# Performance work log

Measured on AMD Instinct MI355X. Metric: run time of the kernel, lower is better.

The kernel has to match this reference:

```python
import jax, jax.numpy as jnp
import numpy as np

# ---- dims (match init_kwargs / input_specs) ----
N = 50000        # nodes
E = 600000       # edges
F_IN = 128       # n_features
HID = 128        # hidden_dims
K = 8            # heads
D_A = 16         # attention dim per head
D_V = 16         # value dim per head
D_M = 64         # max-pool gate dim
CLASSES = 40     # n_classes
LAYERS = 2
SLOPE = 0.1      # negative_slop


def glorot(key, shape):
    lim = jnp.sqrt(6.0 / (shape[-2] + shape[-1]))
    return jax.random.uniform(key, shape, minval=-lim, maxval=lim, dtype=jnp.float32)


def setup_inputs() -> dict:
    key = jax.random.key(0)
    ks = jax.random.split(key, 10)
    x = jax.random.normal(ks[0], (N, F_IN), dtype=jnp.float32)
    edge_index = jax.random.randint(ks[1], (2, E), 0, N, dtype=jnp.int64)
    weight_in = glorot(ks[2], (F_IN, HID))
    weight_out = glorot(ks[3], (HID, CLASSES))
    # per-layer GaANConv params, stacked on leading layer dim
    Wq = glorot(ks[4], (LAYERS, HID, K * D_A))            # query proj
    Wk = glorot(ks[5], (LAYERS, HID, K * D_A))            # key proj
    Wv = glorot(ks[6], (LAYERS, HID, K * D_V))            # value proj
    Wm = glorot(ks[7], (LAYERS, HID, D_M))                # max-pool gate proj
    Wg = glorot(ks[8], (LAYERS, HID + D_M + HID, K))      # gate FC
    Wo = glorot(ks[9], (LAYERS, HID + K * D_V, HID))      # output proj
    return {"x": x, "edge_index": edge_index, "weight_in": weight_in,
            "weight_out": weight_out, "Wq": Wq, "Wk": Wk, "Wv": Wv,
            "Wm": Wm, "Wg": Wg, "Wo": Wo}


def gaan_conv(x, src, dst, wq, wk, wv, wm, wg, wo):
    n = x.shape[0]
    q = (x @ wq).reshape(n, K, D_A)
    k = (x @ wk).reshape(n, K, D_A)
    v = (x @ wv).reshape(n, K, D_V)
    # dot-product attention logits per edge/head: <q_dst, k_src>
    score = jnp.einsum('ekd,ekd->ek', q[dst], k[src])          # [E,K]
    # segment softmax over incoming edges of each dst node
    smax = jax.ops.segment_max(score, dst, num_segments=n)     # [N,K]
    smax = jnp.where(jnp.isfinite(smax), smax, 0.0)            # empty segments -> 0
    ex = jnp.exp(score - smax[dst])
    denom = jax.ops.segment_sum(ex, dst, num_segments=n)
    alpha = ex / (denom[dst] + 1e-16)                          # [E,K]
    agg = jax.ops.segment_sum(alpha[:, :, None] * v[src], dst, num_segments=n)  # [N,K,D_V]
    # gates: sigmoid(FC([x_i, max_j FC_m(x_j), mean_j x_j]))
    m = x @ wm                                                 # [N,D_M]
    maxpool = jax.ops.segment_max(m[src], dst, num_segments=n)
    maxpool = jnp.where(jnp.isfinite(maxpool), maxpool, 0.0)
    deg = jax.ops.segment_sum(jnp.ones((src.shape[0],), x.dtype), dst, num_segments=n)
    meanpool = jax.ops.segment_sum(x[src], dst, num_segments=n) / jnp.maximum(deg, 1.0)[:, None]
    g = jax.nn.sigmoid(jnp.concatenate([x, maxpool, meanpool], axis=1) @ wg)  # [N,K]
    gated = (g[:, :, None] * agg).reshape(n, K * D_V)
    return jnp.concatenate([x, gated], axis=1) @ wo            # [N,HID]


def reference(x, edge_index, weight_in, weight_out, Wq, Wk, Wv, Wm, Wg, Wo):
    src, dst = edge_index[0], edge_index[1]
    h = x @ weight_in
    for i in range(LAYERS):
        h = jax.nn.leaky_relu(
            gaan_conv(h, src, dst, Wq[i], Wk[i], Wv[i], Wm[i], Wg[i], Wo[i]),
            negative_slope=SLOPE)
        # dropout is identity in eval mode
    out = h @ weight_out
    return jax.nn.log_softmax(out, axis=1)
```

## Files before the change

kernel.cpp:

```cpp
#include <hip/hip_runtime.h>
#include <math.h>

#define NNODES 50000
#define NEDGES 600000
#define HIDDIM 128
#define NHEAD 8
#define DM 64
#define NCLS 40
#define FSTR 576

typedef __attribute__((ext_vector_type(8))) short short8;
typedef __attribute__((ext_vector_type(4))) float f32x4;

static __device__ __forceinline__ unsigned short f2bf(float f) {
    unsigned u = __float_as_uint(f);
    unsigned r = (u + 0x7fffu + ((u >> 16) & 1u)) >> 16;
    return (unsigned short)r;
}
static __device__ __forceinline__ float bflo(unsigned u) { return __uint_as_float(u << 16); }
static __device__ __forceinline__ float bfhi(unsigned u) { return __uint_as_float(u & 0xffff0000u); }
static __device__ __forceinline__ float bf2f(unsigned short s) {
    return __uint_as_float(((unsigned)s) << 16);
}

template <int WF32, int WB1, int ACT>
__global__ __launch_bounds__(256) void gemm_mfma(
    const unsigned short* __restrict__ A1, int lda1, int K1,
    const unsigned short* __restrict__ A2, int lda2, int K2,
    const unsigned short* __restrict__ BT,
    float* __restrict__ C, int ldc,
    unsigned short* __restrict__ Cb1, int ldb1, int off1,
    int M, int NN)
{
    const int K = K1 + K2;
    const int l = threadIdx.x & 63, wv = threadIdx.x >> 6;
    const int r = l & 15, g = l >> 4;
    const int row0 = blockIdx.y * 256 + wv * 64;
    const int col0 = blockIdx.x * 64;

    f32x4 acc[4][4] = {};

    for (int k0 = 0; k0 < K; k0 += 32) {
        const unsigned short* Ak;
        int ka, lda;
        if (k0 < K1) { Ak = A1; ka = k0; lda = lda1; }
        else         { Ak = A2; ka = k0 - K1; lda = lda2; }

        short8 a[4], b[4];
#pragma unroll
        for (int m = 0; m < 4; ++m) {
            int row = row0 + m * 16 + r;
            if (row < M)
                a[m] = *reinterpret_cast<const short8*>(Ak + (size_t)row * lda + ka + 8 * g);
            else
                a[m] = short8{0, 0, 0, 0, 0, 0, 0, 0};
        }
#pragma unroll
        for (int n = 0; n < 4; ++n) {
            int col = col0 + n * 16 + r;
            b[n] = *reinterpret_cast<const short8*>(BT + (size_t)col * K + k0 + 8 * g);
        }
#pragma unroll
        for (int m = 0; m < 4; ++m)
#pragma unroll
            for (int n = 0; n < 4; ++n)
                acc[m][n] = __builtin_amdgcn_mfma_f32_16x16x32_bf16(a[m], b[n], acc[m][n], 0, 0, 0);
    }

#pragma unroll
    for (int m = 0; m < 4; ++m) {
#pragma unroll
        for (int j = 0; j < 4; ++j) {
            int row = row0 + m * 16 + 4 * g + j;
            if (row >= M) continue;
#pragma unroll
            for (int n = 0; n < 4; ++n) {
                int col = col0 + n * 16 + r;
                if (col >= NN) continue;
                float vv = acc[m][n][j];
                if (ACT) vv = vv > 0.f ? vv : 0.1f * vv;
                if (WF32) C[(size_t)row * ldc + col] = vv;
                if (WB1)  Cb1[(size_t)row * ldb1 + off1 + col] = f2bf(vv);
            }
        }
    }
}

#define BT_TOTAL 204800
__global__ __launch_bounds__(256) void pack_weights(
    const float* __restrict__ w_in, const float* __restrict__ w_out,
    const float* __restrict__ Wq, const float* __restrict__ Wk,
    const float* __restrict__ Wv, const float* __restrict__ Wm,
    const float* __restrict__ Wo, unsigned short* __restrict__ BT)
{
    int i = blockIdx.x * 256 + threadIdx.x;
    if (i >= BT_TOTAL) return;
    float val;
    if (i < 16384) {
        int c = i >> 7, k = i & 127;
        val = w_in[k * 128 + c];
    } else if (i < 131072) {
        int li = i - 16384;
        int L = li / 57344, t = li % 57344;
        int c = t >> 7, k = t & 127;
        if      (c < 128) val = Wq[L * 16384 + k * 128 + c];
        else if (c < 256) val = Wk[L * 16384 + k * 128 + (c - 128)];
        else if (c < 384) val = Wv[L * 16384 + k * 128 + (c - 256)];
        else              val = Wm[L * 8192  + k * 64  + (c - 384)];
    } else if (i < 196608) {
        int li = i - 131072;
        int L = li / 32768, t = li % 32768;
        int c = t >> 8, k = t & 255;
        val = Wo[L * 32768 + k * 128 + c];
    } else {
        int t = i - 196608;
        int c = t >> 7, k = t & 127;
        val = (c < NCLS) ? w_out[k * NCLS + c] : 0.f;
    }
    BT[i] = f2bf(val);
}

__global__ __launch_bounds__(256) void convert_x_kernel(
    const float* __restrict__ x, unsigned int* __restrict__ xb2)
{
    int i = blockIdx.x * 256 + threadIdx.x;
    if (i >= NNODES * HIDDIM / 2) return;
    float2 f = *reinterpret_cast<const float2*>(x + (size_t)i * 2);
    xb2[i] = (unsigned)f2bf(f.x) | ((unsigned)f2bf(f.y) << 16);
}

__global__ __launch_bounds__(256) void hist_kernel(
    const int* __restrict__ ei, int* __restrict__ degi)
{
    int e = blockIdx.x * 256 + threadIdx.x;
    if (e >= NEDGES) return;
    unsigned d = (unsigned)ei[NEDGES + e]; if (d >= NNODES) d = 0;
    atomicAdd(&degi[d], 1);
}

__global__ __launch_bounds__(1024) void scan_kernel(
    const int* __restrict__ degi, int* __restrict__ rowptr)
{
    __shared__ int sh[1024];
    const int t = threadIdx.x;
    const int chunk = (NNODES + 1023) / 1024;
    int lo = t * chunk, hi = min(lo + chunk, NNODES);
    int s = 0;
    for (int i = lo; i < hi; ++i) s += degi[i];
    sh[t] = s;
    __syncthreads();
    for (int off = 1; off < 1024; off <<= 1) {
        int v = (t >= off) ? sh[t - off] : 0;
        __syncthreads();
        sh[t] += v;
        __syncthreads();
    }
    int excl = (t == 0) ? 0 : sh[t - 1];
    for (int i = lo; i < hi; ++i) {
        rowptr[i] = excl;
        excl += degi[i];
    }
    if (t == 1023) rowptr[NNODES] = excl;
}

__global__ __launch_bounds__(256) void scatter_kernel(
    const int* __restrict__ ei, const int* __restrict__ rowptr,
    int* __restrict__ fill, int* __restrict__ csr_src)
{
    int e = blockIdx.x * 256 + threadIdx.x;
    if (e >= NEDGES) return;
    unsigned s = (unsigned)ei[e];          if (s >= NNODES) s = 0;
    unsigned d = (unsigned)ei[NEDGES + e]; if (d >= NNODES) d = 0;
    int pos = rowptr[d] + atomicAdd(&fill[d], 1);
    csr_src[pos] = (int)s;
}

__global__ __launch_bounds__(256) void fused_edge_kernel(
    const int* __restrict__ rowptr, const int* __restrict__ csr_src,
    const unsigned short* __restrict__ feat, const float* __restrict__ Wg,
    unsigned short* __restrict__ gatedb)
{
    int node = blockIdx.x * 4 + (threadIdx.x >> 6);
    if (node >= NNODES) return;
    const int lane = threadIdx.x & 63;
    const int c2 = lane * 2;

    const int start = rowptr[node], end = rowptr[node + 1];
    const int deg = end - start;

    const unsigned short* frow = feat + (size_t)node * FSTR;
    unsigned qu = *reinterpret_cast<const unsigned*>(frow + c2);
    float qx = bflo(qu), qy = bfhi(qu);

    float mr = -INFINITY, dr = 0.f;
    float a0 = 0.f, a1 = 0.f;
    float ms0 = 0.f, ms1 = 0.f;
    float mm = -INFINITY;

    int p = start;
    for (; p + 2 <= end; p += 2) {
        int s0 = csr_src[p], s1 = csr_src[p + 1];
        const unsigned short* r0 = feat + (size_t)s0 * FSTR;
        const unsigned short* r1 = feat + (size_t)s1 * FSTR;
        unsigned ku0 = *reinterpret_cast<const unsigned*>(r0 + 128 + c2);
        unsigned vu0 = *reinterpret_cast<const unsigned*>(r0 + 256 + c2);
        float    mv0 = bf2f(r0[384 + lane]);
        unsigned hu0 = *reinterpret_cast<const unsigned*>(r0 + 448 + c2);
        unsigned ku1 = *reinterpret_cast<const unsigned*>(r1 + 128 + c2);
        unsigned vu1 = *reinterpret_cast<const unsigned*>(r1 + 256 + c2);
        float    mv1 = bf2f(r1[384 + lane]);
        unsigned hu1 = *reinterpret_cast<const unsigned*>(r1 + 448 + c2);

        float sc0 = qx * bflo(ku0) + qy * bfhi(ku0);
        float sc1 = qx * bflo(ku1) + qy * bfhi(ku1);
        sc0 += __shfl_xor(sc0, 1);  sc1 += __shfl_xor(sc1, 1);
        sc0 += __shfl_xor(sc0, 2);  sc1 += __shfl_xor(sc1, 2);
        sc0 += __shfl_xor(sc0, 4);  sc1 += __shfl_xor(sc1, 4);

        float nm = fmaxf(mr, fmaxf(sc0, sc1));
        float scale = __expf(mr - nm);
        float e0 = __expf(sc0 - nm), e1 = __expf(sc1 - nm);
        dr = dr * scale + e0 + e1;
        a0 = a0 * scale; a0 = fmaf(e0, bflo(vu0), a0); a0 = fmaf(e1, bflo(vu1), a0);
        a1 = a1 * scale; a1 = fmaf(e0, bfhi(vu0), a1); a1 = fmaf(e1, bfhi(vu1), a1);
        mr = nm;

        ms0 += bflo(hu0) + bflo(hu1);
        ms1 += bfhi(hu0) + bfhi(hu1);
        mm = fmaxf(mm, fmaxf(mv0, mv1));
    }
    if (p < end) {
        int s0 = csr_src[p];
        const unsigned short* r0 = feat + (size_t)s0 * FSTR;
        unsigned ku0 = *reinterpret_cast<const unsigned*>(r0 + 128 + c2);
        unsigned vu0 = *reinterpret_cast<const unsigned*>(r0 + 256 + c2);
        float    mv0 = bf2f(r0[384 + lane]);
        unsigned hu0 = *reinterpret_cast<const unsigned*>(r0 + 448 + c2);

        float sc0 = qx * bflo(ku0) + qy * bfhi(ku0);
        sc0 += __shfl_xor(sc0, 1);
        sc0 += __shfl_xor(sc0, 2);
        sc0 += __shfl_xor(sc0, 4);

        float nm = fmaxf(mr, sc0);
        float scale = __expf(mr - nm);
        float e0 = __expf(sc0 - nm);
        dr = dr * scale + e0;
        a0 = fmaf(e0, bflo(vu0), a0 * scale);
        a1 = fmaf(e0, bfhi(vu0), a1 * scale);
        mr = nm;

        ms0 += bflo(hu0);
        ms1 += bfhi(hu0);
        mm = fmaxf(mm, mv0);
    }

    float inv  = 1.f / (dr + 1e-16f);
    float invd = 1.f / fmaxf((float)deg, 1.f);
    if (deg == 0) { mm = 0.f; inv = 0.f; }
    float msx = ms0 * invd, msy = ms1 * invd;

    unsigned hou = *reinterpret_cast<const unsigned*>(frow + 448 + c2);
    float hx = bflo(hou), hy = bfhi(hou);

    const float* w0 = Wg + (size_t)c2 * 8;
    const float* w1 = Wg + (size_t)(c2 + 1) * 8;
    const float* w2 = Wg + (size_t)(128 + lane) * 8;
    const float* w3 = Wg + (size_t)(192 + c2) * 8;
    const float* w4 = Wg + (size_t)(193 + c2) * 8;

    float part[8];
#pragma unroll
    for (int j = 0; j < 8; ++j)
        part[j] = hx * w0[j] + hy * w1[j] + mm * w2[j] + msx * w3[j] + msy * w4[j];
#pragma unroll
    for (int off = 1; off < 64; off <<= 1)
#pragma unroll
        for (int j = 0; j < 8; ++j)
            part[j] += __shfl_xor(part[j], off);

    float g = 1.f / (1.f + __expf(-part[lane >> 3]));
    float o0 = g * a0 * inv, o1 = g * a1 * inv;
    unsigned outu = (unsigned)f2bf(o0) | ((unsigned)f2bf(o1) << 16);
    *reinterpret_cast<unsigned*>(gatedb + (size_t)node * HIDDIM + c2) = outu;
}

__global__ __launch_bounds__(256) void logsoftmax_kernel(float* __restrict__ out)
{
    int gt = blockIdx.x * 256 + threadIdx.x;
    int wid = gt >> 6;
    int lane = threadIdx.x & 63;
    if (wid >= NNODES) return;
    float* row = out + (size_t)wid * NCLS;
    float x = (lane < NCLS) ? row[lane] : -INFINITY;
    float mx = x;
#pragma unroll
    for (int off = 32; off; off >>= 1) mx = fmaxf(mx, __shfl_xor(mx, off));
    float ex = (lane < NCLS) ? __expf(x - mx) : 0.f;
    float sm = ex;
#pragma unroll
    for (int off = 32; off; off >>= 1) sm += __shfl_xor(sm, off);
    float lse = mx + logf(sm);
    if (lane < NCLS) row[lane] = x - lse;
}

static inline int cdiv(int a, int b) { return (a + b - 1) / b; }

extern "C" void kernel_launch(void* const* d_in, const int* in_sizes, int n_in,
                              void* d_out, int out_size, void* d_ws, size_t ws_size,
                              hipStream_t stream)
{
    const float* x     = (const float*)d_in[0];
    const int*   ei    = (const int*)d_in[1];
    const float* w_in  = (const float*)d_in[2];
    const float* w_out = (const float*)d_in[3];
    const float* Wq    = (const float*)d_in[4];
    const float* Wk    = (const float*)d_in[5];
    const float* Wv    = (const float*)d_in[6];
    const float* Wm    = (const float*)d_in[7];
    const float* Wg    = (const float*)d_in[8];
    const float* Wo    = (const float*)d_in[9];
    float* out = (float*)d_out;

    const size_t NF = NNODES;
    unsigned short* xb     = (unsigned short*)d_ws;
    unsigned short* feat0  = xb    + NF * 128;
    unsigned short* feat1  = feat0 + NF * FSTR;
    unsigned short* gatedb = feat1 + NF * FSTR;
    unsigned short* BTpool = gatedb + NF * 128;
    int* rowptr  = (int*)(BTpool + BT_TOTAL);
    int* degi    = rowptr + (NNODES + 1);
    int* fill    = degi + NNODES;
    int* csr_src = fill + NNODES;

    const unsigned short* BTin    = BTpool;
    const unsigned short* BTqkvm0 = BTpool + 16384;
    const unsigned short* BTqkvm1 = BTpool + 73728;
    const unsigned short* BTo0    = BTpool + 131072;
    const unsigned short* BTo1    = BTpool + 163840;
    const unsigned short* BTout   = BTpool + 196608;

    pack_weights<<<cdiv(BT_TOTAL, 256), 256, 0, stream>>>(
        w_in, w_out, Wq, Wk, Wv, Wm, Wo, BTpool);
    convert_x_kernel<<<cdiv(NNODES * HIDDIM / 2, 256), 256, 0, stream>>>(
        x, (unsigned int*)xb);
    hipMemsetAsync(degi, 0, 2 * NNODES * sizeof(int), stream);
    hist_kernel<<<cdiv(NEDGES, 256), 256, 0, stream>>>(ei, degi);
    scan_kernel<<<1, 1024, 0, stream>>>(degi, rowptr);
    scatter_kernel<<<cdiv(NEDGES, 256), 256, 0, stream>>>(ei, rowptr, fill, csr_src);

    const dim3 g128(2, cdiv(NNODES, 256));
    const dim3 g448(7, cdiv(NNODES, 256));
    const dim3 g40 (1, cdiv(NNODES, 256));

    gemm_mfma<0, 1, 0><<<g128, 256, 0, stream>>>(
        xb, 128, 128, nullptr, 0, 0, BTin,
        nullptr, 0, feat0, FSTR, 448, NNODES, 128);

    unsigned short* featA = feat0;
    unsigned short* featB = feat1;
    for (int L = 0; L < 2; ++L) {
        const unsigned short* btq = L ? BTqkvm1 : BTqkvm0;
        const unsigned short* bto = L ? BTo1 : BTo0;
        const float* wg = Wg + (size_t)L * 320 * 8;

        gemm_mfma<0, 1, 0><<<g448, 256, 0, stream>>>(
            featA + 448, FSTR, 128, nullptr, 0, 0, btq,
            nullptr, 0, featA, FSTR, 0, NNODES, 448);

        fused_edge_kernel<<<cdiv(NNODES, 4), 256, 0, stream>>>(
            rowptr, csr_src, featA, wg, gatedb);

        gemm_mfma<0, 1, 1><<<g128, 256, 0, stream>>>(
            featA + 448, FSTR, 128, gatedb, 128, 128, bto,
            nullptr, 0, featB, FSTR, 448, NNODES, 128);

        unsigned short* t = featA; featA = featB; featB = t;
    }

    gemm_mfma<1, 0, 0><<<g40, 256, 0, stream>>>(
        featA + 448, FSTR, 128, nullptr, 0, 0, BTout,
        out, NCLS, nullptr, 0, 0, NNODES, NCLS);
    logsoftmax_kernel<<<cdiv(NNODES * 64, 256), 256, 0, stream>>>(out);
}
```

Baseline: 551.8 us.

## Precompute mean-pool gate projection per node and halve GEMM row tile

Because the mean-pool gate term is linear, it is rewritten as the mean over neighbours of a per-node 8-wide projection h·Wg_mean. That projection is appended as extra output columns of the QKVM GEMM, so the edge kernel gathers 8 bf16 values per edge instead of a 128-wide hidden row. This is meant to cut per-edge gather traffic in the memory-bound edge kernel. Separately, the GEMM tile drops from 256 to 128 rows per block, which launches more blocks at the cost of less B-operand reuse. The projection is stored in bf16 before averaging, which adds a small rounding difference.

```diff
diff --git a/kernel.cpp b/kernel.cpp
--- a/kernel.cpp
+++ b/kernel.cpp
@@ -7,7 +7,12 @@
 #define NHEAD 8
 #define DM 64
 #define NCLS 40
-#define FSTR 576
+#define FSTR 584
+#define OFF_K 128
+#define OFF_V 256
+#define OFF_M 384
+#define OFF_HG 448
+#define OFF_H 456
 
 typedef __attribute__((ext_vector_type(8))) short short8;
 typedef __attribute__((ext_vector_type(4))) float f32x4;
@@ -35,10 +40,10 @@
     const int K = K1 + K2;
     const int l = threadIdx.x & 63, wv = threadIdx.x >> 6;
     const int r = l & 15, g = l >> 4;
-    const int row0 = blockIdx.y * 256 + wv * 64;
+    const int row0 = blockIdx.y * 128 + wv * 32;
     const int col0 = blockIdx.x * 64;
 
-    f32x4 acc[4][4] = {};
+    f32x4 acc[2][4] = {};
 
     for (int k0 = 0; k0 < K; k0 += 32) {
         const unsigned short* Ak;
@@ -46,9 +51,9 @@
         if (k0 < K1) { Ak = A1; ka = k0; lda = lda1; }
         else         { Ak = A2; ka = k0 - K1; lda = lda2; }
 
-        short8 a[4], b[4];
-#pragma unroll
-        for (int m = 0; m < 4; ++m) {
+        short8 a[2], b[4];
+#pragma unroll
+        for (int m = 0; m < 2; ++m) {
             int row = row0 + m * 16 + r;
             if (row < M)
                 a[m] = *reinterpret_cast<const short8*>(Ak + (size_t)row * lda + ka + 8 * g);
@@ -61,14 +66,14 @@
             b[n] = *reinterpret_cast<const short8*>(BT + (size_t)col * K + k0 + 8 * g);
         }
 #pragma unroll
-        for (int m = 0; m < 4; ++m)
+        for (int m = 0; m < 2; ++m)
 #pragma unroll
             for (int n = 0; n < 4; ++n)
                 acc[m][n] = __builtin_amdgcn_mfma_f32_16x16x32_bf16(a[m], b[n], acc[m][n], 0, 0, 0);
     }
 
 #pragma unroll
-    for (int m = 0; m < 4; ++m) {
+    for (int m = 0; m < 2; ++m) {
 #pragma unroll
         for (int j = 0; j < 4; ++j) {
             int row = row0 + m * 16 + 4 * g + j;
@@ -86,12 +91,13 @@
     }
 }
 
-#define BT_TOTAL 204800
+#define BT_TOTAL 206848
 __global__ __launch_bounds__(256) void pack_weights(
     const float* __restrict__ w_in, const float* __restrict__ w_out,
     const float* __restrict__ Wq, const float* __restrict__ Wk,
     const float* __restrict__ Wv, const float* __restrict__ Wm,
-    const float* __restrict__ Wo, unsigned short* __restrict__ BT)
+    const float* __restrict__ Wg, const float* __restrict__ Wo,
+    unsigned short* __restrict__ BT)
 {
     int i = blockIdx.x * 256 + threadIdx.x;
     if (i >= BT_TOTAL) return;
@@ -99,21 +105,22 @@
     if (i < 16384) {
         int c = i >> 7, k = i & 127;
         val = w_in[k * 128 + c];
-    } else if (i < 131072) {
+    } else if (i < 133120) {
         int li = i - 16384;
-        int L = li / 57344, t = li % 57344;
+        int L = li / 58368, t = li % 58368;
         int c = t >> 7, k = t & 127;
         if      (c < 128) val = Wq[L * 16384 + k * 128 + c];
         else if (c < 256) val = Wk[L * 16384 + k * 128 + (c - 128)];
         else if (c < 384) val = Wv[L * 16384 + k * 128 + (c - 256)];
-        else              val = Wm[L * 8192  + k * 64  + (c - 384)];
-    } else if (i < 196608) {
-        int li = i - 131072;
+        else if (c < 448) val = Wm[L * 8192  + k * 64  + (c - 384)];
+        else              val = Wg[L * 2560 + (192 + k) * 8 + (c - 448)];
+    } else if (i < 198656) {
+        int li = i - 133120;
         int L = li / 32768, t = li % 32768;
         int c = t >> 8, k = t & 255;
         val = Wo[L * 32768 + k * 128 + c];
     } else {
-        int t = i - 196608;
+        int t = i - 198656;
         int c = t >> 7, k = t & 127;
         val = (c < NCLS) ? w_out[k * NCLS + c] : 0.f;
     }
@@ -184,6 +191,7 @@
     if (node >= NNODES) return;
     const int lane = threadIdx.x & 63;
     const int c2 = lane * 2;
+    const int j0 = lane & 7;
 
     const int start = rowptr[node], end = rowptr[node + 1];
     const int deg = end - start;
@@ -194,7 +202,7 @@
 
     float mr = -INFINITY, dr = 0.f;
     float a0 = 0.f, a1 = 0.f;
-    float ms0 = 0.f, ms1 = 0.f;
+    float hgs = 0.f;
     float mm = -INFINITY;
 
     int p = start;
@@ -202,14 +210,14 @@
         int s0 = csr_src[p], s1 = csr_src[p + 1];
         const unsigned short* r0 = feat + (size_t)s0 * FSTR;
         const unsigned short* r1 = feat + (size_t)s1 * FSTR;
-        unsigned ku0 = *reinterpret_cast<const unsigned*>(r0 + 128 + c2);
-        unsigned vu0 = *reinterpret_cast<const unsigned*>(r0 + 256 + c2);
-        float    mv0 = bf2f(r0[384 + lane]);
-        unsigned hu0 = *reinterpret_cast<const unsigned*>(r0 + 448 + c2);
-        unsigned ku1 = *reinterpret_cast<const unsigned*>(r1 + 128 + c2);
-        unsigned vu1 = *reinterpret_cast<const unsigned*>(r1 + 256 + c2);
-        float    mv1 = bf2f(r1[384 + lane]);
-        unsigned hu1 = *reinterpret_cast<const unsigned*>(r1 + 448 + c2);
+        unsigned ku0 = *reinterpret_cast<const unsigned*>(r0 + OFF_K + c2);
+        unsigned vu0 = *reinterpret_cast<const unsigned*>(r0 + OFF_V + c2);
+        float    mv0 = bf2f(r0[OFF_M + lane]);
+        float    hg0 = bf2f(r0[OFF_HG + j0]);
+        unsigned ku1 = *reinterpret_cast<const unsigned*>(r1 + OFF_K + c2);
+        unsigned vu1 = *reinterpret_cast<const unsigned*>(r1 + OFF_V + c2);
+        float    mv1 = bf2f(r1[OFF_M + lane]);
+        float    hg1 = bf2f(r1[OFF_HG + j0]);
 
         float sc0 = qx * bflo(ku0) + qy * bfhi(ku0);
         float sc1 = qx * bflo(ku1) + qy * bfhi(ku1);
@@ -225,17 +233,16 @@
         a1 = a1 * scale; a1 = fmaf(e0, bfhi(vu0), a1); a1 = fmaf(e1, bfhi(vu1), a1);
         mr = nm;
 
-        ms0 += bflo(hu0) + bflo(hu1);
-        ms1 += bfhi(hu0) + bfhi(hu1);
+        hgs += hg0 + hg1;
         mm = fmaxf(mm, fmaxf(mv0, mv1));
     }
     if (p < end) {
         int s0 = csr_src[p];
         const unsigned short* r0 = feat + (size_t)s0 * FSTR;
-        unsigned ku0 = *reinterpret_cast<const unsigned*>(r0 + 128 + c2);
-        unsigned vu0 = *reinterpret_cast<const unsigned*>(r0 + 256 + c2);
-        float    mv0 = bf2f(r0[384 + lane]);
-        unsigned hu0 = *reinterpret_cast<const unsigned*>(r0 + 448 + c2);
+        unsigned ku0 = *reinterpret_cast<const unsigned*>(r0 + OFF_K + c2);
+        unsigned vu0 = *reinterpret_cast<const unsigned*>(r0 + OFF_V + c2);
+        float    mv0 = bf2f(r0[OFF_M + lane]);
+        float    hg0 = bf2f(r0[OFF_HG + j0]);
 
         float sc0 = qx * bflo(ku0) + qy * bfhi(ku0);
         sc0 += __shfl_xor(sc0, 1);
@@ -250,37 +257,34 @@
         a1 = fmaf(e0, bfhi(vu0), a1 * scale);
         mr = nm;
 
-        ms0 += bflo(hu0);
-        ms1 += bfhi(hu0);
+        hgs += hg0;
         mm = fmaxf(mm, mv0);
     }
 
     float inv  = 1.f / (dr + 1e-16f);
     float invd = 1.f / fmaxf((float)deg, 1.f);
     if (deg == 0) { mm = 0.f; inv = 0.f; }
-    float msx = ms0 * invd, msy = ms1 * invd;
-
-    unsigned hou = *reinterpret_cast<const unsigned*>(frow + 448 + c2);
+
+    unsigned hou = *reinterpret_cast<const unsigned*>(frow + OFF_H + c2);
     float hx = bflo(hou), hy = bfhi(hou);
 
     const float* w0 = Wg + (size_t)c2 * 8;
     const float* w1 = Wg + (size_t)(c2 + 1) * 8;
     const float* w2 = Wg + (size_t)(128 + lane) * 8;
-    const float* w3 = Wg + (size_t)(192 + c2) * 8;
-    const float* w4 = Wg + (size_t)(193 + c2) * 8;
 
     float part[8];
 #pragma unroll
     for (int j = 0; j < 8; ++j)
-        part[j] = hx * w0[j] + hy * w1[j] + mm * w2[j] + msx * w3[j] + msy * w4[j];
+        part[j] = hx * w0[j] + hy * w1[j] + mm * w2[j];
 #pragma unroll
     for (int off = 1; off < 64; off <<= 1)
 #pragma unroll
         for (int j = 0; j < 8; ++j)
             part[j] += __shfl_xor(part[j], off);
 
-    float g = 1.f / (1.f + __expf(-part[lane >> 3]));
-    float o0 = g * a0 * inv, o1 = g * a1 * inv;
+    float mc = __shfl(hgs, lane >> 3);
+    float gg = 1.f / (1.f + __expf(-(part[lane >> 3] + mc * invd)));
+    float o0 = gg * a0 * inv, o1 = gg * a1 * inv;
     unsigned outu = (unsigned)f2bf(o0) | ((unsigned)f2bf(o1) << 16);
     *reinterpret_cast<unsigned*>(gatedb + (size_t)node * HIDDIM + c2) = outu;
 }
@@ -335,13 +339,13 @@
 
     const unsigned short* BTin    = BTpool;
     const unsigned short* BTqkvm0 = BTpool + 16384;
-    const unsigned short* BTqkvm1 = BTpool + 73728;
-    const unsigned short* BTo0    = BTpool + 131072;
-    const unsigned short* BTo1    = BTpool + 163840;
-    const unsigned short* BTout   = BTpool + 196608;
+    const unsigned short* BTqkvm1 = BTpool + 74752;
+    const unsigned short* BTo0    = BTpool + 133120;
+    const unsigned short* BTo1    = BTpool + 165888;
+    const unsigned short* BTout   = BTpool + 198656;
 
     pack_weights<<<cdiv(BT_TOTAL, 256), 256, 0, stream>>>(
-        w_in, w_out, Wq, Wk, Wv, Wm, Wo, BTpool);
+        w_in, w_out, Wq, Wk, Wv, Wm, Wg, Wo, BTpool);
     convert_x_kernel<<<cdiv(NNODES * HIDDIM / 2, 256), 256, 0, stream>>>(
         x, (unsigned int*)xb);
     hipMemsetAsync(degi, 0, 2 * NNODES * sizeof(int), stream);
@@ -349,13 +353,13 @@
     scan_kernel<<<1, 1024, 0, stream>>>(degi, rowptr);
     scatter_kernel<<<cdiv(NEDGES, 256), 256, 0, stream>>>(ei, rowptr, fill, csr_src);
 
-    const dim3 g128(2, cdiv(NNODES, 256));
-    const dim3 g448(7, cdiv(NNODES, 256));
-    const dim3 g40 (1, cdiv(NNODES, 256));
+    const dim3 g128(2, cdiv(NNODES, 128));
+    const dim3 g456(8, cdiv(NNODES, 128));
+    const dim3 g40 (1, cdiv(NNODES, 128));
 
     gemm_mfma<0, 1, 0><<<g128, 256, 0, stream>>>(
         xb, 128, 128, nullptr, 0, 0, BTin,
-        nullptr, 0, feat0, FSTR, 448, NNODES, 128);
+        nullptr, 0, feat0, FSTR, OFF_H, NNODES, 128);
 
     unsigned short* featA = feat0;
     unsigned short* featB = feat1;
@@ -364,22 +368,22 @@
         const unsigned short* bto = L ? BTo1 : BTo0;
         const float* wg = Wg + (size_t)L * 320 * 8;
 
-        gemm_mfma<0, 1, 0><<<g448, 256, 0, stream>>>(
-            featA + 448, FSTR, 128, nullptr, 0, 0, btq,
-            nullptr, 0, featA, FSTR, 0, NNODES, 448);
+        gemm_mfma<0, 1, 0><<<g456, 256, 0, stream>>>(
+            featA + OFF_H, FSTR, 128, nullptr, 0, 0, btq,
+            nullptr, 0, featA, FSTR, 0, NNODES, 456);
 
         fused_edge_kernel<<<cdiv(NNODES, 4), 256, 0, stream>>>(
             rowptr, csr_src, featA, wg, gatedb);
 
         gemm_mfma<0, 1, 1><<<g128, 256, 0, stream>>>(
-            featA + 448, FSTR, 128, gatedb, 128, 128, bto,
-            nullptr, 0, featB, FSTR, 448, NNODES, 128);
+            featA + OFF_H, FSTR, 128, gatedb, 128, 128, bto,
+            nullptr, 0, featB, FSTR, OFF_H, NNODES, 128);
 
         unsigned short* t = featA; featA = featB; featB = t;
     }
 
     gemm_mfma<1, 0, 0><<<g40, 256, 0, stream>>>(
-        featA + 448, FSTR, 128, nullptr, 0, 0, BTout,
+        featA + OFF_H, FSTR, 128, nullptr, 0, 0, BTout,
         out, NCLS, nullptr, 0, 0, NNODES, NCLS);
     logsoftmax_kernel<<<cdiv(NNODES * 64, 256), 256, 0, stream>>>(out);
 }
```

Measured after the change: 556.5 us. About the same (+0.8%).
